# Optimization experiments

Measured on AMD Instinct MI355X. Metric: run time of the kernel, lower is better.

The kernel has to match this reference:

```python
import jax, jax.numpy as jnp
import numpy as np

CUTOFF = 3  # cutoff_freq default in low_pass_filter


def _low_pass(x):
    # full 2D FFT over (H, W), keep only the 4 corner blocks of size CUTOFF
    H, W = x.shape[-2], x.shape[-1]
    f = jnp.fft.fftn(x, axes=(-2, -1))
    mask = jnp.zeros((H, W), dtype=x.dtype)
    c = CUTOFF
    mask = mask.at[:c, :c].set(1).at[:c, -c:].set(1).at[-c:, :c].set(1).at[-c:, -c:].set(1)
    return jnp.abs(jnp.fft.ifftn(f * mask, axes=(-2, -1)))


def setup_inputs() -> dict:
    key = jax.random.key(0)
    k_x, k_w1, k_b1, k_w2, k_b2 = jax.random.split(key, 5)
    n_feat = 8
    B, C, H, W = 32, 3, 512, 512
    x = jax.random.uniform(k_x, (B, C, H, W), dtype=jnp.float32)
    # 1x1 convs == channel-mixing matrices; kaiming-ish scale
    w1 = jax.random.normal(k_w1, (n_feat, C), dtype=jnp.float32) * (1.0 / np.sqrt(C))
    b1 = jax.random.normal(k_b1, (n_feat,), dtype=jnp.float32) * 0.01
    w2 = jax.random.normal(k_w2, (C, n_feat), dtype=jnp.float32) * (1.0 / np.sqrt(n_feat))
    b2 = jax.random.normal(k_b2, (C,), dtype=jnp.float32) * 0.01
    return {"x": x, "w1": w1, "b1": b1, "w2": w2, "b2": b2}


def reference(x, w1, b1, w2, b2):
    lp = _low_pass(x)                                        # [B,3,H,W]
    h = jax.nn.relu(jnp.einsum('bchw,fc->bfhw', lp, w1) + b1[None, :, None, None])
    y = jnp.einsum('bfhw,cf->bchw', h, w2) + b2[None, :, None, None]
    return jnp.clip(y + lp, 0.0, 1.0)
```

## Files before the change

### kernel.cpp

```cpp
#include <hip/hip_runtime.h>
#include <math.h>


#define WS_TS 0
#define WS_PP 8192
#define WS_A  65536
constexpr int NPART = 8;

#define CJ1 0.99992470183914450299f
#define CJ2 0.99969881869620422012f
#define CJ3 0.99932238458834954375f
#define CJ4 0.99879545620517239271f
#define SJ1 0.01227153828571992539f
#define SJ2 0.02454122852291228803f
#define SJ3 0.03680722294135883171f
#define SJ4 0.04906767432741801425f

__global__ __launch_bounds__(256) void k_colsum(const float* __restrict__ x,
                                                float* __restrict__ ws) {
    __shared__ float tile[3 * 2048];
    float* A = ws + WS_A;
    int img = blockIdx.x >> 3;
    int hgrp = blockIdx.x & 7;
    int t = threadIdx.x;
    int wave = t >> 6;
    int lane = t & 63;
    const float* xb = x + (size_t)img * 262144 + (size_t)(hgrp * 64) * 512;

    auto stage = [&](int b, int tt) {
#pragma unroll
        for (int j = 0; j < 2; ++j) {
            int c = wave * 2 + j;
            const float* g = xb + (size_t)tt * 2048 + c * 256 + lane * 4;
            float* l = &tile[b * 2048 + c * 256];
            __builtin_amdgcn_global_load_lds(
                (const __attribute__((address_space(1))) void*)g,
                (__attribute__((address_space(3))) void*)l, 16, 0, 0);
        }
    };

    const float TH = 6.28318530717958647692f / 512.0f;
    float bc, bs;
    sincosf(TH * (float)(hgrp * 64), &bs, &bc);
    const float CJr[4] = {1.f, CJ1, CJ2, CJ3};
    const float SJr[4] = {0.f, SJ1, SJ2, SJ3};

    float aA[7], aB[7];
#pragma unroll
    for (int c = 0; c < 7; ++c) { aA[c] = 0.f; aB[c] = 0.f; }

    stage(0, 0);
    stage(1, 1);
    asm volatile("s_waitcnt vmcnt(2)" ::: "memory");
    asm volatile("s_barrier" ::: "memory");

    int bcur = 0;
    for (int tt = 0; tt < 16; ++tt) {
        int bnext = bcur + 2; if (bnext >= 3) bnext -= 3;
        if (tt + 2 < 16) stage(bnext, tt + 2);

        const float* tb = &tile[bcur * 2048];
#pragma unroll
        for (int j = 0; j < 4; ++j) {
            float c1 = bc * CJr[j] - bs * SJr[j];
            float s1 = bs * CJr[j] + bc * SJr[j];
            float c2 = c1 * c1 - s1 * s1;
            float s2 = 2.f * c1 * s1;
            float c3 = c1 * c2 - s1 * s2;
            float s3 = s1 * c2 + c1 * s2;
            float xa = tb[j * 512 + t];
            float xc = tb[j * 512 + t + 256];
            aA[0] += xa;
            aA[1] = fmaf(xa, c1, aA[1]);  aA[2] = fmaf(-xa, s1, aA[2]);
            aA[3] = fmaf(xa, c2, aA[3]);  aA[4] = fmaf(-xa, s2, aA[4]);
            aA[5] = fmaf(xa, c3, aA[5]);  aA[6] = fmaf(-xa, s3, aA[6]);
            aB[0] += xc;
            aB[1] = fmaf(xc, c1, aB[1]);  aB[2] = fmaf(-xc, s1, aB[2]);
            aB[3] = fmaf(xc, c2, aB[3]);  aB[4] = fmaf(-xc, s2, aB[4]);
            aB[5] = fmaf(xc, c3, aB[5]);  aB[6] = fmaf(-xc, s3, aB[6]);
        }
        {
            float nb = bc * CJ4 - bs * SJ4;
            bs = bs * CJ4 + bc * SJ4;
            bc = nb;
        }

        if (tt + 2 < 16) asm volatile("s_waitcnt vmcnt(2)" ::: "memory");
        else             asm volatile("s_waitcnt vmcnt(0)" ::: "memory");
        asm volatile("s_barrier" ::: "memory");
        bcur = bcur + 1; if (bcur >= 3) bcur -= 3;
    }

    float* Ab = A + (((size_t)img * NPART + hgrp) * 8) * 512;
    const int pl[7] = {0, 2, 3, 4, 5, 6, 7};
#pragma unroll
    for (int c = 0; c < 7; ++c) {
        Ab[(size_t)pl[c] * 512 + t]       = aA[c];
        Ab[(size_t)pl[c] * 512 + t + 256] = aB[c];
    }
    Ab[(size_t)1 * 512 + t]       = 0.f;
    Ab[(size_t)1 * 512 + t + 256] = 0.f;
}

__global__ __launch_bounds__(256) void k_proj(float* __restrict__ ws) {
    int t = threadIdx.x;
    const float TH = 6.28318530717958647692f / 512.0f;
    if (blockIdx.x == 768) {
        const int mv[6] = {0, 1, 2, -3, -2, -1};
        for (int h = t; h < 512; h += 256) {
            float* tsp = ws + WS_TS + h * 12;
#pragma unroll
            for (int i = 0; i < 6; ++i) {
                int r = ((mv[i] * h) % 512 + 512) & 511;
                float s, c;
                sincosf(TH * (float)r, &s, &c);
                tsp[2 * i] = c; tsp[2 * i + 1] = s;
            }
        }
        return;
    }
    __shared__ float As[8][64];
    const float* A = ws + WS_A;
    float* Pp = ws + WS_PP;
    int img = blockIdx.x >> 3;
    int seg = blockIdx.x & 7;

    {
        int plane = t >> 5;
        int wl = (t & 31) * 2;
        float2 L[8];
#pragma unroll
        for (int hg = 0; hg < NPART; ++hg)
            L[hg] = *(const float2*)(A + (((size_t)img * NPART + hg) * 8 + plane) * 512 + seg * 64 + wl);
        float ax = 0.f, ay = 0.f;
#pragma unroll
        for (int hg = 0; hg < NPART; ++hg) { ax += L[hg].x; ay += L[hg].y; }
        As[plane][wl] = ax;
        As[plane][wl + 1] = ay;
    }
    __syncthreads();

    if (t < 28) {
        int k = t / 7, mi = t % 7;
        float m = (float)(mi - 3);
        float cm, sm, pc, ps;
        sincosf(-m * TH, &sm, &cm);
        sincosf(-m * TH * (float)(seg * 64), &ps, &pc);
        const float* Ar_ = &As[2 * k][0];
        const float* Ai_ = &As[2 * k + 1][0];
        float pre = 0.f, pim = 0.f;
#pragma unroll 4
        for (int j = 0; j < 64; ++j) {
            float Ar = Ar_[j], Ai = Ai_[j];
            pre += Ar * pc - Ai * ps;
            pim += Ar * ps + Ai * pc;
            float n = pc * cm - ps * sm;
            ps = ps * cm + pc * sm;
            pc = n;
        }
        float* o = Pp + ((size_t)img * 8 + seg) * 56;
        o[t * 2] = pre;
        o[t * 2 + 1] = pim;
    }
}

__global__ __launch_bounds__(256) void k_out(const float* __restrict__ ws,
                                             const float* __restrict__ w1,
                                             const float* __restrict__ b1,
                                             const float* __restrict__ w2,
                                             const float* __restrict__ b2,
                                             float* __restrict__ out) {
    const float* tabS = ws + WS_TS;
    const float* Pp = ws + WS_PP;
    __shared__ float F_lds[3][56];
    __shared__ float T[4][3][12];
    int t = threadIdx.x;
    int blk = blockIdx.x;
    int b = blk >> 7;
    int h0 = (blk & 127) << 2;

    if (t < 168) {
        int c = t / 56, comp = t % 56;
        const float* pp = Pp + ((size_t)(b * 3 + c) * 8) * 56 + comp;
        float s = 0.f;
#pragma unroll
        for (int g = 0; g < 8; ++g) s += pp[g * 56];
        F_lds[c][comp] = s;
    }

    float rw1[8][3], rb1[8], rw2[3][8], rb2[3];
#pragma unroll
    for (int f_ = 0; f_ < 8; ++f_) {
        rb1[f_] = b1[f_];
#pragma unroll
        for (int c = 0; c < 3; ++c) rw1[f_][c] = w1[f_ * 3 + c];
    }
#pragma unroll
    for (int c = 0; c < 3; ++c) {
        rb2[c] = b2[c];
#pragma unroll
        for (int f_ = 0; f_ < 8; ++f_) rw2[c][f_] = w2[c * 8 + f_];
    }
    __syncthreads();

    if (t < 72) {
        int rl = t / 18, rem = t % 18;
        int c = rem / 6, kc = rem % 6;
        int h = h0 + rl;
        const float* th = tabS + h * 12;
        int m_kc = (kc < 3) ? kc : kc - 6;
        const float inv = 1.0f / (512.0f * 512.0f);
        float tre = 0.f, tim = 0.f;
#pragma unroll
        for (int kr = 0; kr < 6; ++kr) {
            int kk, mi; float csign;
            if (kr < 3) { kk = kr;     mi = m_kc + 3; csign =  1.f; }
            else        { kk = 6 - kr; mi = 3 - m_kc; csign = -1.f; }
            int pair = kk * 7 + mi;
            float fr = F_lds[c][pair * 2] * inv;
            float fi = F_lds[c][pair * 2 + 1] * csign * inv;
            float cc = th[kr * 2], ss = th[kr * 2 + 1];
            tre += fr * cc - fi * ss;
            tim += fr * ss + fi * cc;
        }
        T[rl][c][kc * 2]     = tre;
        T[rl][c][kc * 2 + 1] = tim;
    }
    __syncthreads();

    int rl = t >> 6, lane = t & 63;
    int h = h0 + rl;
    float A0r[3], A0i[3], U1r[3], U1i[3], V1r[3], V1i[3];
    float U2r[3], U2i[3], V2r[3], V2i[3], Br[3], Bi[3];
#pragma unroll
    for (int c = 0; c < 3; ++c) {
        const float* Tc = T[rl][c];
        A0r[c] = Tc[0];  A0i[c] = Tc[1];
        float t1r = Tc[2],  t1i = Tc[3];
        float t2r = Tc[4],  t2i = Tc[5];
        float bmr = Tc[6],  bmi = Tc[7];
        float m2r = Tc[8],  m2i = Tc[9];
        float m1r = Tc[10], m1i = Tc[11];
        U1r[c] = t1r + m1r; U1i[c] = t1i + m1i;
        V1r[c] = t1r - m1r; V1i[c] = t1i - m1i;
        U2r[c] = t2r + m2r; U2i[c] = t2i + m2i;
        V2r[c] = t2r - m2r; V2i[c] = t2i - m2i;
        Br[c] = bmr; Bi[c] = bmi;
    }
    const float* tw = tabS + lane * 12;
    float c1 = tw[2], s1 = tw[3];
    float c2 = tw[4], s2 = tw[5];
    float c3 = tw[6], s3 = -tw[7];
    const float K = 0.70710678118654752440f;
    float* ob = out + ((size_t)(b * 3) * 512 + h) * 512;

#pragma unroll
    for (int j = 0; j < 8; ++j) {
        int w = lane + 64 * j;
        float lp[3];
#pragma unroll
        for (int c = 0; c < 3; ++c) {
            float re = A0r[c] + U1r[c] * c1 - V1i[c] * s1
                              + U2r[c] * c2 - V2i[c] * s2
                              + Br[c] * c3 + Bi[c] * s3;
            float im = A0i[c] + U1i[c] * c1 + V1r[c] * s1
                              + U2i[c] * c2 + V2r[c] * s2
                              + Bi[c] * c3 - Br[c] * s3;
            lp[c] = sqrtf(re * re + im * im);
        }
        float hid[8];
#pragma unroll
        for (int f_ = 0; f_ < 8; ++f_) {
            float v = rb1[f_] + lp[0] * rw1[f_][0] + lp[1] * rw1[f_][1] + lp[2] * rw1[f_][2];
            hid[f_] = fmaxf(v, 0.0f);
        }
#pragma unroll
        for (int c = 0; c < 3; ++c) {
            float y = rb2[c] + lp[c];
#pragma unroll
            for (int f_ = 0; f_ < 8; ++f_) y += hid[f_] * rw2[c][f_];
            y = fminf(fmaxf(y, 0.0f), 1.0f);
            ob[(size_t)c * 262144 + w] = y;
        }
        if (j < 7) {
            float nc1 = K * (c1 - s1), ns1 = K * (c1 + s1);
            float nc2 = -s2,           ns2 = c2;
            float nc3 = -K * (c3 + s3), ns3 = K * (c3 - s3);
            c1 = nc1; s1 = ns1; c2 = nc2; s2 = ns2; c3 = nc3; s3 = ns3;
        }
    }
}

extern "C" void kernel_launch(void* const* d_in, const int* in_sizes, int n_in,
                              void* d_out, int out_size, void* d_ws, size_t ws_size,
                              hipStream_t stream) {
    const float* x  = (const float*)d_in[0];
    const float* w1 = (const float*)d_in[1];
    const float* b1 = (const float*)d_in[2];
    const float* w2 = (const float*)d_in[3];
    const float* b2 = (const float*)d_in[4];
    float* out = (float*)d_out;
    float* ws = (float*)d_ws;

    hipLaunchKernelGGL(k_colsum, dim3(96 * NPART), dim3(256), 0, stream, x, ws);
    hipLaunchKernelGGL(k_proj, dim3(769), dim3(256), 0, stream, ws);
    hipLaunchKernelGGL(k_out, dim3(4096), dim3(256), 0, stream, ws, w1, b1, w2, b2, out);
}
```

Before: 63.99 us.

## Merge three stages into one role-dispatched kernel, pipelined across image chunks

Merges the column-sum, projection and output kernels into one kernel that picks its role from the block index. The work is split into four chunks of 24 images, and six launches stagger the stages so that column sums for one chunk run alongside projection and output for earlier chunks. The aim is to overlap the read-heavy input pass with the write-heavy output pass and cut idle tail time between dependent kernels. In exchange there are more launches, and every block reserves the full 24KB shared buffer, which may reduce occupancy for the output role.

```diff
diff --git a/kernel.cpp b/kernel.cpp
--- a/kernel.cpp
+++ b/kernel.cpp
@@ -16,277 +16,282 @@
 #define SJ3 0.03680722294135883171f
 #define SJ4 0.04906767432741801425f
 
-__global__ __launch_bounds__(256) void k_colsum(const float* __restrict__ x,
-                                                float* __restrict__ ws) {
-    __shared__ float tile[3 * 2048];
-    float* A = ws + WS_A;
-    int img = blockIdx.x >> 3;
-    int hgrp = blockIdx.x & 7;
-    int t = threadIdx.x;
-    int wave = t >> 6;
-    int lane = t & 63;
-    const float* xb = x + (size_t)img * 262144 + (size_t)(hgrp * 64) * 512;
-
-    auto stage = [&](int b, int tt) {
-#pragma unroll
-        for (int j = 0; j < 2; ++j) {
-            int c = wave * 2 + j;
-            const float* g = xb + (size_t)tt * 2048 + c * 256 + lane * 4;
-            float* l = &tile[b * 2048 + c * 256];
-            __builtin_amdgcn_global_load_lds(
-                (const __attribute__((address_space(1))) void*)g,
-                (__attribute__((address_space(3))) void*)l, 16, 0, 0);
-        }
-    };
-
-    const float TH = 6.28318530717958647692f / 512.0f;
-    float bc, bs;
-    sincosf(TH * (float)(hgrp * 64), &bs, &bc);
-    const float CJr[4] = {1.f, CJ1, CJ2, CJ3};
-    const float SJr[4] = {0.f, SJ1, SJ2, SJ3};
-
-    float aA[7], aB[7];
-#pragma unroll
-    for (int c = 0; c < 7; ++c) { aA[c] = 0.f; aB[c] = 0.f; }
-
-    stage(0, 0);
-    stage(1, 1);
-    asm volatile("s_waitcnt vmcnt(2)" ::: "memory");
-    asm volatile("s_barrier" ::: "memory");
-
-    int bcur = 0;
-    for (int tt = 0; tt < 16; ++tt) {
-        int bnext = bcur + 2; if (bnext >= 3) bnext -= 3;
-        if (tt + 2 < 16) stage(bnext, tt + 2);
-
-        const float* tb = &tile[bcur * 2048];
-#pragma unroll
-        for (int j = 0; j < 4; ++j) {
-            float c1 = bc * CJr[j] - bs * SJr[j];
-            float s1 = bs * CJr[j] + bc * SJr[j];
-            float c2 = c1 * c1 - s1 * s1;
-            float s2 = 2.f * c1 * s1;
-            float c3 = c1 * c2 - s1 * s2;
-            float s3 = s1 * c2 + c1 * s2;
-            float xa = tb[j * 512 + t];
-            float xc = tb[j * 512 + t + 256];
-            aA[0] += xa;
-            aA[1] = fmaf(xa, c1, aA[1]);  aA[2] = fmaf(-xa, s1, aA[2]);
-            aA[3] = fmaf(xa, c2, aA[3]);  aA[4] = fmaf(-xa, s2, aA[4]);
-            aA[5] = fmaf(xa, c3, aA[5]);  aA[6] = fmaf(-xa, s3, aA[6]);
-            aB[0] += xc;
-            aB[1] = fmaf(xc, c1, aB[1]);  aB[2] = fmaf(-xc, s1, aB[2]);
-            aB[3] = fmaf(xc, c2, aB[3]);  aB[4] = fmaf(-xc, s2, aB[4]);
-            aB[5] = fmaf(xc, c3, aB[5]);  aB[6] = fmaf(-xc, s3, aB[6]);
-        }
-        {
-            float nb = bc * CJ4 - bs * SJ4;
-            bs = bs * CJ4 + bc * SJ4;
-            bc = nb;
-        }
-
-        if (tt + 2 < 16) asm volatile("s_waitcnt vmcnt(2)" ::: "memory");
-        else             asm volatile("s_waitcnt vmcnt(0)" ::: "memory");
-        asm volatile("s_barrier" ::: "memory");
-        bcur = bcur + 1; if (bcur >= 3) bcur -= 3;
-    }
-
-    float* Ab = A + (((size_t)img * NPART + hgrp) * 8) * 512;
-    const int pl[7] = {0, 2, 3, 4, 5, 6, 7};
-#pragma unroll
-    for (int c = 0; c < 7; ++c) {
-        Ab[(size_t)pl[c] * 512 + t]       = aA[c];
-        Ab[(size_t)pl[c] * 512 + t + 256] = aB[c];
-    }
-    Ab[(size_t)1 * 512 + t]       = 0.f;
-    Ab[(size_t)1 * 512 + t + 256] = 0.f;
-}
-
-__global__ __launch_bounds__(256) void k_proj(float* __restrict__ ws) {
-    int t = threadIdx.x;
-    const float TH = 6.28318530717958647692f / 512.0f;
-    if (blockIdx.x == 768) {
-        const int mv[6] = {0, 1, 2, -3, -2, -1};
-        for (int h = t; h < 512; h += 256) {
-            float* tsp = ws + WS_TS + h * 12;
-#pragma unroll
-            for (int i = 0; i < 6; ++i) {
-                int r = ((mv[i] * h) % 512 + 512) & 511;
-                float s, c;
-                sincosf(TH * (float)r, &s, &c);
-                tsp[2 * i] = c; tsp[2 * i + 1] = s;
-            }
-        }
-        return;
-    }
-    __shared__ float As[8][64];
-    const float* A = ws + WS_A;
-    float* Pp = ws + WS_PP;
-    int img = blockIdx.x >> 3;
-    int seg = blockIdx.x & 7;
-
-    {
-        int plane = t >> 5;
-        int wl = (t & 31) * 2;
-        float2 L[8];
-#pragma unroll
-        for (int hg = 0; hg < NPART; ++hg)
-            L[hg] = *(const float2*)(A + (((size_t)img * NPART + hg) * 8 + plane) * 512 + seg * 64 + wl);
-        float ax = 0.f, ay = 0.f;
-#pragma unroll
-        for (int hg = 0; hg < NPART; ++hg) { ax += L[hg].x; ay += L[hg].y; }
-        As[plane][wl] = ax;
-        As[plane][wl + 1] = ay;
-    }
-    __syncthreads();
-
-    if (t < 28) {
-        int k = t / 7, mi = t % 7;
-        float m = (float)(mi - 3);
-        float cm, sm, pc, ps;
-        sincosf(-m * TH, &sm, &cm);
-        sincosf(-m * TH * (float)(seg * 64), &ps, &pc);
-        const float* Ar_ = &As[2 * k][0];
-        const float* Ai_ = &As[2 * k + 1][0];
-        float pre = 0.f, pim = 0.f;
-#pragma unroll 4
-        for (int j = 0; j < 64; ++j) {
-            float Ar = Ar_[j], Ai = Ai_[j];
-            pre += Ar * pc - Ai * ps;
-            pim += Ar * ps + Ai * pc;
-            float n = pc * cm - ps * sm;
-            ps = ps * cm + pc * sm;
-            pc = n;
-        }
-        float* o = Pp + ((size_t)img * 8 + seg) * 56;
-        o[t * 2] = pre;
-        o[t * 2 + 1] = pim;
-    }
-}
-
-__global__ __launch_bounds__(256) void k_out(const float* __restrict__ ws,
+__global__ __launch_bounds__(256) void k_mix(const float* __restrict__ x,
                                              const float* __restrict__ w1,
                                              const float* __restrict__ b1,
                                              const float* __restrict__ w2,
                                              const float* __restrict__ b2,
-                                             float* __restrict__ out) {
-    const float* tabS = ws + WS_TS;
-    const float* Pp = ws + WS_PP;
-    __shared__ float F_lds[3][56];
-    __shared__ float T[4][3][12];
+                                             float* __restrict__ out,
+                                             float* __restrict__ ws,
+                                             int csImg0, int csN,
+                                             int pjImg0, int pjN,
+                                             int outB0, int outN, int tab) {
+    __shared__ float smem[6144];
+    int bid = blockIdx.x;
     int t = threadIdx.x;
-    int blk = blockIdx.x;
-    int b = blk >> 7;
-    int h0 = (blk & 127) << 2;
-
-    if (t < 168) {
-        int c = t / 56, comp = t % 56;
-        const float* pp = Pp + ((size_t)(b * 3 + c) * 8) * 56 + comp;
-        float s = 0.f;
-#pragma unroll
-        for (int g = 0; g < 8; ++g) s += pp[g * 56];
-        F_lds[c][comp] = s;
+    const float TH = 6.28318530717958647692f / 512.0f;
+
+    if (bid < csN) {
+        float* tile = smem;
+        float* A = ws + WS_A;
+        int img = csImg0 + (bid >> 3);
+        int hgrp = bid & 7;
+        int wave = t >> 6;
+        int lane = t & 63;
+        const float* xb = x + (size_t)img * 262144 + (size_t)(hgrp * 64) * 512;
+
+        auto stage = [&](int b, int tt) {
+#pragma unroll
+            for (int j = 0; j < 2; ++j) {
+                int c = wave * 2 + j;
+                const float* g = xb + (size_t)tt * 2048 + c * 256 + lane * 4;
+                float* l = &tile[b * 2048 + c * 256];
+                __builtin_amdgcn_global_load_lds(
+                    (const __attribute__((address_space(1))) void*)g,
+                    (__attribute__((address_space(3))) void*)l, 16, 0, 0);
+            }
+        };
+
+        float bc, bs;
+        sincosf(TH * (float)(hgrp * 64), &bs, &bc);
+        const float CJr[4] = {1.f, CJ1, CJ2, CJ3};
+        const float SJr[4] = {0.f, SJ1, SJ2, SJ3};
+
+        float aA[7], aB[7];
+#pragma unroll
+        for (int c = 0; c < 7; ++c) { aA[c] = 0.f; aB[c] = 0.f; }
+
+        stage(0, 0);
+        stage(1, 1);
+        asm volatile("s_waitcnt vmcnt(2)" ::: "memory");
+        asm volatile("s_barrier" ::: "memory");
+
+        int bcur = 0;
+        for (int tt = 0; tt < 16; ++tt) {
+            int bnext = bcur + 2; if (bnext >= 3) bnext -= 3;
+            if (tt + 2 < 16) stage(bnext, tt + 2);
+
+            const float* tb = &tile[bcur * 2048];
+#pragma unroll
+            for (int j = 0; j < 4; ++j) {
+                float c1 = bc * CJr[j] - bs * SJr[j];
+                float s1 = bs * CJr[j] + bc * SJr[j];
+                float c2 = c1 * c1 - s1 * s1;
+                float s2 = 2.f * c1 * s1;
+                float c3 = c1 * c2 - s1 * s2;
+                float s3 = s1 * c2 + c1 * s2;
+                float xa = tb[j * 512 + t];
+                float xc = tb[j * 512 + t + 256];
+                aA[0] += xa;
+                aA[1] = fmaf(xa, c1, aA[1]);  aA[2] = fmaf(-xa, s1, aA[2]);
+                aA[3] = fmaf(xa, c2, aA[3]);  aA[4] = fmaf(-xa, s2, aA[4]);
+                aA[5] = fmaf(xa, c3, aA[5]);  aA[6] = fmaf(-xa, s3, aA[6]);
+                aB[0] += xc;
+                aB[1] = fmaf(xc, c1, aB[1]);  aB[2] = fmaf(-xc, s1, aB[2]);
+                aB[3] = fmaf(xc, c2, aB[3]);  aB[4] = fmaf(-xc, s2, aB[4]);
+                aB[5] = fmaf(xc, c3, aB[5]);  aB[6] = fmaf(-xc, s3, aB[6]);
+            }
+            {
+                float nb = bc * CJ4 - bs * SJ4;
+                bs = bs * CJ4 + bc * SJ4;
+                bc = nb;
+            }
+            if (tt + 2 < 16) asm volatile("s_waitcnt vmcnt(2)" ::: "memory");
+            else             asm volatile("s_waitcnt vmcnt(0)" ::: "memory");
+            asm volatile("s_barrier" ::: "memory");
+            bcur = bcur + 1; if (bcur >= 3) bcur -= 3;
+        }
+
+        float* Ab = A + (((size_t)img * NPART + hgrp) * 8) * 512;
+        const int pl[7] = {0, 2, 3, 4, 5, 6, 7};
+#pragma unroll
+        for (int c = 0; c < 7; ++c) {
+            Ab[(size_t)pl[c] * 512 + t]       = aA[c];
+            Ab[(size_t)pl[c] * 512 + t + 256] = aB[c];
+        }
+        Ab[(size_t)1 * 512 + t]       = 0.f;
+        Ab[(size_t)1 * 512 + t + 256] = 0.f;
+        return;
     }
 
-    float rw1[8][3], rb1[8], rw2[3][8], rb2[3];
-#pragma unroll
-    for (int f_ = 0; f_ < 8; ++f_) {
-        rb1[f_] = b1[f_];
-#pragma unroll
-        for (int c = 0; c < 3; ++c) rw1[f_][c] = w1[f_ * 3 + c];
+    if (bid < csN + pjN) {
+        float (*As)[64] = (float (*)[64])smem;
+        const float* A = ws + WS_A;
+        float* Pp = ws + WS_PP;
+        int r = bid - csN;
+        int img = pjImg0 + (r >> 3);
+        int seg = r & 7;
+        {
+            int plane = t >> 5;
+            int wl = (t & 31) * 2;
+            float ax = 0.f, ay = 0.f;
+#pragma unroll
+            for (int hg = 0; hg < NPART; ++hg) {
+                float2 v = *(const float2*)(A + (((size_t)img * NPART + hg) * 8 + plane) * 512 + seg * 64 + wl);
+                ax += v.x; ay += v.y;
+            }
+            As[plane][wl] = ax;
+            As[plane][wl + 1] = ay;
+        }
+        __syncthreads();
+        if (t < 28) {
+            int k = t / 7, mi = t % 7;
+            float m = (float)(mi - 3);
+            float cm, sm, pc, ps;
+            sincosf(-m * TH, &sm, &cm);
+            sincosf(-m * TH * (float)(seg * 64), &ps, &pc);
+            const float* Ar_ = &As[2 * k][0];
+            const float* Ai_ = &As[2 * k + 1][0];
+            float pre = 0.f, pim = 0.f;
+#pragma unroll 4
+            for (int j = 0; j < 64; ++j) {
+                float Ar = Ar_[j], Ai = Ai_[j];
+                pre += Ar * pc - Ai * ps;
+                pim += Ar * ps + Ai * pc;
+                float n = pc * cm - ps * sm;
+                ps = ps * cm + pc * sm;
+                pc = n;
+            }
+            float* o = Pp + ((size_t)img * 8 + seg) * 56;
+            o[t * 2] = pre;
+            o[t * 2 + 1] = pim;
+        }
+        return;
     }
-#pragma unroll
-    for (int c = 0; c < 3; ++c) {
-        rb2[c] = b2[c];
-#pragma unroll
-        for (int f_ = 0; f_ < 8; ++f_) rw2[c][f_] = w2[c * 8 + f_];
+
+    if (tab && bid == csN + pjN + outN) {
+        const int mv[6] = {0, 1, 2, -3, -2, -1};
+        for (int h = t; h < 512; h += 256) {
+            float* tsp = ws + WS_TS + h * 12;
+#pragma unroll
+            for (int i = 0; i < 6; ++i) {
+                int rr = ((mv[i] * h) % 512 + 512) & 511;
+                float s, c;
+                sincosf(TH * (float)rr, &s, &c);
+                tsp[2 * i] = c; tsp[2 * i + 1] = s;
+            }
+        }
+        return;
     }
-    __syncthreads();
-
-    if (t < 72) {
-        int rl = t / 18, rem = t % 18;
-        int c = rem / 6, kc = rem % 6;
+
+    {
+        const float* tabS = ws + WS_TS;
+        const float* Pp = ws + WS_PP;
+        float (*F_lds)[56] = (float (*)[56])smem;
+        float (*T)[3][12] = (float (*)[3][12])(smem + 168);
+        int r = bid - csN - pjN;
+        int b = outB0 + (r >> 7);
+        int h0 = (r & 127) << 2;
+
+        if (t < 168) {
+            int c = t / 56, comp = t % 56;
+            const float* pp = Pp + ((size_t)(b * 3 + c) * 8) * 56 + comp;
+            float s = 0.f;
+#pragma unroll
+            for (int g = 0; g < 8; ++g) s += pp[g * 56];
+            F_lds[c][comp] = s;
+        }
+
+        float rw1[8][3], rb1[8], rw2[3][8], rb2[3];
+#pragma unroll
+        for (int f_ = 0; f_ < 8; ++f_) {
+            rb1[f_] = b1[f_];
+#pragma unroll
+            for (int c = 0; c < 3; ++c) rw1[f_][c] = w1[f_ * 3 + c];
+        }
+#pragma unroll
+        for (int c = 0; c < 3; ++c) {
+            rb2[c] = b2[c];
+#pragma unroll
+            for (int f_ = 0; f_ < 8; ++f_) rw2[c][f_] = w2[c * 8 + f_];
+        }
+        __syncthreads();
+
+        if (t < 72) {
+            int rl = t / 18, rem = t % 18;
+            int c = rem / 6, kc = rem % 6;
+            int h = h0 + rl;
+            const float* th = tabS + h * 12;
+            int m_kc = (kc < 3) ? kc : kc - 6;
+            const float inv = 1.0f / (512.0f * 512.0f);
+            float tre = 0.f, tim = 0.f;
+#pragma unroll
+            for (int kr = 0; kr < 6; ++kr) {
+                int kk, mi; float csign;
+                if (kr < 3) { kk = kr;     mi = m_kc + 3; csign =  1.f; }
+                else        { kk = 6 - kr; mi = 3 - m_kc; csign = -1.f; }
+                int pair = kk * 7 + mi;
+                float fr = F_lds[c][pair * 2] * inv;
+                float fi = F_lds[c][pair * 2 + 1] * csign * inv;
+                float cc = th[kr * 2], ss = th[kr * 2 + 1];
+                tre += fr * cc - fi * ss;
+                tim += fr * ss + fi * cc;
+            }
+            T[rl][c][kc * 2]     = tre;
+            T[rl][c][kc * 2 + 1] = tim;
+        }
+        __syncthreads();
+
+        int rl = t >> 6, lane = t & 63;
         int h = h0 + rl;
-        const float* th = tabS + h * 12;
-        int m_kc = (kc < 3) ? kc : kc - 6;
-        const float inv = 1.0f / (512.0f * 512.0f);
-        float tre = 0.f, tim = 0.f;
-#pragma unroll
-        for (int kr = 0; kr < 6; ++kr) {
-            int kk, mi; float csign;
-            if (kr < 3) { kk = kr;     mi = m_kc + 3; csign =  1.f; }
-            else        { kk = 6 - kr; mi = 3 - m_kc; csign = -1.f; }
-            int pair = kk * 7 + mi;
-            float fr = F_lds[c][pair * 2] * inv;
-            float fi = F_lds[c][pair * 2 + 1] * csign * inv;
-            float cc = th[kr * 2], ss = th[kr * 2 + 1];
-            tre += fr * cc - fi * ss;
-            tim += fr * ss + fi * cc;
-        }
-        T[rl][c][kc * 2]     = tre;
-        T[rl][c][kc * 2 + 1] = tim;
-    }
-    __syncthreads();
-
-    int rl = t >> 6, lane = t & 63;
-    int h = h0 + rl;
-    float A0r[3], A0i[3], U1r[3], U1i[3], V1r[3], V1i[3];
-    float U2r[3], U2i[3], V2r[3], V2i[3], Br[3], Bi[3];
-#pragma unroll
-    for (int c = 0; c < 3; ++c) {
-        const float* Tc = T[rl][c];
-        A0r[c] = Tc[0];  A0i[c] = Tc[1];
-        float t1r = Tc[2],  t1i = Tc[3];
-        float t2r = Tc[4],  t2i = Tc[5];
-        float bmr = Tc[6],  bmi = Tc[7];
-        float m2r = Tc[8],  m2i = Tc[9];
-        float m1r = Tc[10], m1i = Tc[11];
-        U1r[c] = t1r + m1r; U1i[c] = t1i + m1i;
-        V1r[c] = t1r - m1r; V1i[c] = t1i - m1i;
-        U2r[c] = t2r + m2r; U2i[c] = t2i + m2i;
-        V2r[c] = t2r - m2r; V2i[c] = t2i - m2i;
-        Br[c] = bmr; Bi[c] = bmi;
-    }
-    const float* tw = tabS + lane * 12;
-    float c1 = tw[2], s1 = tw[3];
-    float c2 = tw[4], s2 = tw[5];
-    float c3 = tw[6], s3 = -tw[7];
-    const float K = 0.70710678118654752440f;
-    float* ob = out + ((size_t)(b * 3) * 512 + h) * 512;
-
-#pragma unroll
-    for (int j = 0; j < 8; ++j) {
-        int w = lane + 64 * j;
-        float lp[3];
+        float A0r[3], A0i[3], U1r[3], U1i[3], V1r[3], V1i[3];
+        float U2r[3], U2i[3], V2r[3], V2i[3], Br[3], Bi[3];
 #pragma unroll
         for (int c = 0; c < 3; ++c) {
-            float re = A0r[c] + U1r[c] * c1 - V1i[c] * s1
-                              + U2r[c] * c2 - V2i[c] * s2
-                              + Br[c] * c3 + Bi[c] * s3;
-            float im = A0i[c] + U1i[c] * c1 + V1r[c] * s1
-                              + U2i[c] * c2 + V2r[c] * s2
-                              + Bi[c] * c3 - Br[c] * s3;
-            lp[c] = sqrtf(re * re + im * im);
-        }
-        float hid[8];
-#pragma unroll
-        for (int f_ = 0; f_ < 8; ++f_) {
-            float v = rb1[f_] + lp[0] * rw1[f_][0] + lp[1] * rw1[f_][1] + lp[2] * rw1[f_][2];
-            hid[f_] = fmaxf(v, 0.0f);
-        }
-#pragma unroll
-        for (int c = 0; c < 3; ++c) {
-            float y = rb2[c] + lp[c];
-#pragma unroll
-            for (int f_ = 0; f_ < 8; ++f_) y += hid[f_] * rw2[c][f_];
-            y = fminf(fmaxf(y, 0.0f), 1.0f);
-            ob[(size_t)c * 262144 + w] = y;
-        }
-        if (j < 7) {
-            float nc1 = K * (c1 - s1), ns1 = K * (c1 + s1);
-            float nc2 = -s2,           ns2 = c2;
-            float nc3 = -K * (c3 + s3), ns3 = K * (c3 - s3);
-            c1 = nc1; s1 = ns1; c2 = nc2; s2 = ns2; c3 = nc3; s3 = ns3;
+            const float* Tc = T[rl][c];
+            A0r[c] = Tc[0];  A0i[c] = Tc[1];
+            float t1r = Tc[2],  t1i = Tc[3];
+            float t2r = Tc[4],  t2i = Tc[5];
+            float bmr = Tc[6],  bmi = Tc[7];
+            float m2r = Tc[8],  m2i = Tc[9];
+            float m1r = Tc[10], m1i = Tc[11];
+            U1r[c] = t1r + m1r; U1i[c] = t1i + m1i;
+            V1r[c] = t1r - m1r; V1i[c] = t1i - m1i;
+            U2r[c] = t2r + m2r; U2i[c] = t2i + m2i;
+            V2r[c] = t2r - m2r; V2i[c] = t2i - m2i;
+            Br[c] = bmr; Bi[c] = bmi;
+        }
+        const float* tw = tabS + lane * 12;
+        float c1 = tw[2], s1 = tw[3];
+        float c2 = tw[4], s2 = tw[5];
+        float c3 = tw[6], s3 = -tw[7];
+        const float K = 0.70710678118654752440f;
+        float* ob = out + ((size_t)(b * 3) * 512 + h) * 512;
+
+#pragma unroll
+        for (int j = 0; j < 8; ++j) {
+            int w = lane + 64 * j;
+            float lp[3];
+#pragma unroll
+            for (int c = 0; c < 3; ++c) {
+                float re = A0r[c] + U1r[c] * c1 - V1i[c] * s1
+                                  + U2r[c] * c2 - V2i[c] * s2
+                                  + Br[c] * c3 + Bi[c] * s3;
+                float im = A0i[c] + U1i[c] * c1 + V1r[c] * s1
+                                  + U2i[c] * c2 + V2r[c] * s2
+                                  + Bi[c] * c3 - Br[c] * s3;
+                lp[c] = sqrtf(re * re + im * im);
+            }
+            float hid[8];
+#pragma unroll
+            for (int f_ = 0; f_ < 8; ++f_) {
+                float v = rb1[f_] + lp[0] * rw1[f_][0] + lp[1] * rw1[f_][1] + lp[2] * rw1[f_][2];
+                hid[f_] = fmaxf(v, 0.0f);
+            }
+#pragma unroll
+            for (int c = 0; c < 3; ++c) {
+                float y = rb2[c] + lp[c];
+#pragma unroll
+                for (int f_ = 0; f_ < 8; ++f_) y += hid[f_] * rw2[c][f_];
+                y = fminf(fmaxf(y, 0.0f), 1.0f);
+                ob[(size_t)c * 262144 + w] = y;
+            }
+            if (j < 7) {
+                float nc1 = K * (c1 - s1), ns1 = K * (c1 + s1);
+                float nc2 = -s2,           ns2 = c2;
+                float nc3 = -K * (c3 + s3), ns3 = K * (c3 - s3);
+                c1 = nc1; s1 = ns1; c2 = nc2; s2 = ns2; c3 = nc3; s3 = ns3;
+            }
         }
     }
 }
@@ -302,7 +307,16 @@
     float* out = (float*)d_out;
     float* ws = (float*)d_ws;
 
-    hipLaunchKernelGGL(k_colsum, dim3(96 * NPART), dim3(256), 0, stream, x, ws);
-    hipLaunchKernelGGL(k_proj, dim3(769), dim3(256), 0, stream, ws);
-    hipLaunchKernelGGL(k_out, dim3(4096), dim3(256), 0, stream, ws, w1, b1, w2, b2, out);
+    auto L = [&](int csI, int csN, int pjI, int pjN, int ob0, int oN, int tab) {
+        int grid = csN + pjN + oN + (tab ? 1 : 0);
+        hipLaunchKernelGGL(k_mix, dim3(grid), dim3(256), 0, stream,
+                           x, w1, b1, w2, b2, out, ws,
+                           csI, csN, pjI, pjN, ob0, oN, tab);
+    };
+    L( 0, 192,  0,   0,  0,    0, 1);
+    L(24, 192,  0, 192,  0,    0, 0);
+    L(48, 192, 24, 192,  0, 1024, 0);
+    L(72, 192, 48, 192,  8, 1024, 0);
+    L( 0,   0, 72, 192, 16, 1024, 0);
+    L( 0,   0,  0,   0, 24, 1024, 0);
 }
```

New measurement: 78.27 us. 22.3% more time.
